# Optimization experiments

Hardware: AMD Instinct MI355X
Metric: run time of the kernel (lower is better)

Reference implementation:

```python
import jax, jax.numpy as jnp
import numpy as np

N = 4096
DK = 128   # d_k == d_e == d_h (required by gate shapes in KAG)
DH = 128
DR = 64
DE = 128
NHEADS = 3
ALPHA = 0.2
NEG_INF = -9e15


def _xavier(k, shape, gain=1.414):
    fan_in, fan_out = shape[-2], shape[-1]
    limit = gain * np.sqrt(6.0 / (fan_in + fan_out))
    return jax.random.uniform(k, shape, minval=-limit, maxval=limit, dtype=jnp.float32)


def setup_inputs() -> dict:
    key = jax.random.key(0)
    ks = jax.random.split(key, 16)
    x = jax.random.normal(ks[0], (N, DK), dtype=jnp.float32)
    adj = (jax.random.uniform(ks[1], (N, N)) < 0.01).astype(jnp.float32)
    adj = jnp.maximum(adj, jnp.eye(N, dtype=jnp.float32))
    e_t = jax.random.normal(ks[2], (N, DE), dtype=jnp.float32)
    r_t = jax.random.normal(ks[3], (N, DR), dtype=jnp.float32)
    prev_h = jax.random.normal(ks[4], (N, DH), dtype=jnp.float32)
    # GAT params: NHEADS input heads + one output head
    W_heads = _xavier(ks[5], (NHEADS, DK, DH))
    a_heads = _xavier(ks[6], (NHEADS, 2 * DH, 1))
    W_out = _xavier(ks[7], (NHEADS * DH, DH))
    a_out = _xavier(ks[8], (2 * DH, 1))
    # KAG + OutputLayer linear params (stored [in, out])
    din_kag = DK + DR + DH  # 320
    Wq_w = _xavier(ks[9], (din_kag, DK), gain=1.0)
    Wq_b = jnp.zeros((DK,), jnp.float32)
    Wh_w = _xavier(ks[10], (din_kag, DH), gain=1.0)
    Wh_b = jnp.zeros((DH,), jnp.float32)
    din_out = DK + DE + DH  # 384
    Wp_w = _xavier(ks[11], (din_out, DH), gain=1.0)
    Wp_b = jnp.zeros((DH,), jnp.float32)
    return {"x": x, "adj": adj, "e_t": e_t, "r_t": r_t, "prev_h": prev_h,
            "W_heads": W_heads, "a_heads": a_heads, "W_out": W_out, "a_out": a_out,
            "Wq_w": Wq_w, "Wq_b": Wq_b, "Wh_w": Wh_w, "Wh_b": Wh_b,
            "Wp_w": Wp_w, "Wp_b": Wp_b}


def _gat_layer(h, adj, W, a, concat):
    # h: [N, Fin], W: [Fin, F], a: [2F, 1]
    Wh = h @ W                       # [N, F]
    F_ = W.shape[1]
    # a^T [Wh_i ; Wh_j] == (Wh a1)_i + (Wh a2)_j  -- identical math, no [N,N,2F]
    f1 = Wh @ a[:F_]                 # [N, 1]
    f2 = Wh @ a[F_:]                 # [N, 1]
    e = jax.nn.leaky_relu(f1 + f2.T, negative_slope=ALPHA)  # [N, N]
    e = jnp.where(adj > 0, e, NEG_INF)
    att = jax.nn.softmax(e, axis=1)  # dropout(p=0.6) is identity in eval mode
    h_prime = att @ Wh               # [N, F]
    return jax.nn.elu(h_prime) if concat else h_prime


def reference(x, adj, e_t, r_t, prev_h, W_heads, a_heads, W_out, a_out,
              Wq_w, Wq_b, Wh_w, Wh_b, Wp_w, Wp_b):
    # --- GAT ---
    heads = jax.vmap(lambda W, a: _gat_layer(x, adj, W, a, True))(W_heads, a_heads)  # [H,N,DH]
    h_cat = jnp.transpose(heads, (1, 0, 2)).reshape(N, NHEADS * DH)
    h_gat = jax.nn.elu(_gat_layer(h_cat, adj, W_out, a_out, False))  # [N, DH]
    # --- KAG gated update (x_t := e_t per CEKT.forward call) ---
    comb = jnp.concatenate([e_t, r_t, prev_h], axis=1)  # [N, DE+DR+DH]
    g = jax.nn.sigmoid(comb @ Wq_w + Wq_b)
    cand = jnp.tanh(comb @ Wh_w + Wh_b)
    h_t = (1.0 - g) * prev_h + g * cand                 # [N, DH]
    # --- Output layer (kc_t := x per CEKT.forward call) ---
    comb2 = jnp.concatenate([h_t, e_t, x], axis=1)      # [N, DH+DE+DK]
    y_t = jax.nn.sigmoid(comb2 @ Wp_w + Wp_b)           # [N, DH]
    return y_t
```

## Files before the change

kernel.cpp:

```cpp
#include <hip/hip_runtime.h>
#include <hip/hip_bf16.h>


typedef short s16x8 __attribute__((ext_vector_type(8)));
typedef float f32x4 __attribute__((ext_vector_type(4)));

constexpr int NKQ = 10;
constexpr int NKP = 12;

__device__ __forceinline__ ushort bf16_rne(float f) {
    union { float f; uint u; } a; a.f = f;
    return (ushort)((a.u + 0x7FFFu + ((a.u >> 16) & 1u)) >> 16);
}
__device__ __forceinline__ float fsigmoid(float z) {
    return 1.0f / (1.0f + __expf(-z));
}
__device__ __forceinline__ float ftanh(float z) {
    const float a = fabsf(z);
    const float t = __expf(-2.0f * a);
    const float r = (1.0f - t) / (1.0f + t);
    return copysignf(r, z);
}

__device__ __forceinline__ s16x8 ldfrag(const float* __restrict__ W,
                                        int s, int krow, int colW) {
    const float* p = W + (s * 32 + krow) * 128 + colW;
    union { ushort u[8]; s16x8 v; } r;
#pragma unroll
    for (int j = 0; j < 8; ++j)
        r.u[j] = bf16_rne(p[j * 128]);
    return r.v;
}

__global__ __launch_bounds__(1024, 1) void cekt_fused(
    const float* __restrict__ x,
    const float* __restrict__ e_t,
    const float* __restrict__ r_t,
    const float* __restrict__ prev_h,
    const float* __restrict__ Wq,
    const float* __restrict__ Wh,
    const float* __restrict__ Wp,
    const float* __restrict__ bq,
    const float* __restrict__ bh,
    const float* __restrict__ bp,
    float* __restrict__ out)
{
    __shared__ alignas(16) ushort A1h[NKQ * 64 * 8];
    __shared__ alignas(16) ushort A2h[NKP * 64 * 8];
    __shared__ f32x4 p1g[8][64], p1c[8][64], p2y[8][64];

    const int t = threadIdx.x;
    const int row0 = blockIdx.x * 16;
    const int w = t >> 6, lane = t & 63;
    const int ct = w & 7, kh = w >> 3;
    const int krow = (lane >> 4) * 8;
    const int colW = ct * 16 + (lane & 15);
    const int colL = lane & 15, rg = lane >> 4;
    const int col = ct * 16 + colL;

    const int sbeg = kh * 5;
    s16x8 hq[5], hc[5];
#pragma unroll
    for (int si = 0; si < 5; ++si) {
        hq[si] = ldfrag(Wq, sbeg + si, krow, colW);
        hc[si] = ldfrag(Wh, sbeg + si, krow, colW);
    }

    for (int i = t; i < 1280; i += 1024) {
        const int row = i / 80, kq4 = i - row * 80;
        const int k0 = kq4 * 4;
        float4 v;
        if (k0 < 128)      v = *(const float4*)&e_t[(row0 + row) * 128 + k0];
        else if (k0 < 192) v = *(const float4*)&r_t[(row0 + row) * 64 + (k0 - 128)];
        else               v = *(const float4*)&prev_h[(row0 + row) * 128 + (k0 - 192)];
        const int s = k0 >> 5, q = (k0 >> 3) & 3, j0 = k0 & 7;
        const int base = (s * 64 + q * 16 + row) * 8 + j0;
        ushort hi4[4];
        hi4[0] = bf16_rne(v.x); hi4[1] = bf16_rne(v.y);
        hi4[2] = bf16_rne(v.z); hi4[3] = bf16_rne(v.w);
        *(uint2*)&A1h[base] = *(const uint2*)hi4;
    }
    {
        const int row = t >> 6, kr = t & 63;
        const int k0 = 128 + kr * 4;
        const float4 v = (k0 < 256)
            ? *(const float4*)&e_t[(row0 + row) * 128 + (k0 - 128)]
            : *(const float4*)&x[(row0 + row) * 128 + (k0 - 256)];
        const int s = k0 >> 5, q = (k0 >> 3) & 3, j0 = k0 & 7;
        const int base = (s * 64 + q * 16 + row) * 8 + j0;
        ushort hi4[4];
        hi4[0] = bf16_rne(v.x); hi4[1] = bf16_rne(v.y);
        hi4[2] = bf16_rne(v.z); hi4[3] = bf16_rne(v.w);
        *(uint2*)&A2h[base] = *(const uint2*)hi4;
    }
    __syncthreads();

    f32x4 gacc = {0, 0, 0, 0}, cacc = {0, 0, 0, 0};
#pragma unroll
    for (int si = 0; si < 5; ++si) {
        const int s = sbeg + si;
        const s16x8 aH = *(const s16x8*)&A1h[(s * 64 + lane) * 8];
        gacc = __builtin_amdgcn_mfma_f32_16x16x32_bf16(aH, hq[si], gacc, 0, 0, 0);
        cacc = __builtin_amdgcn_mfma_f32_16x16x32_bf16(aH, hc[si], cacc, 0, 0, 0);
    }

    s16x8 pH[6];
    float ph4[4];
    if (kh) {
        p1g[ct][lane] = gacc;
        p1c[ct][lane] = cacc;
#pragma unroll
        for (int si = 0; si < 6; ++si)
            pH[si] = ldfrag(Wp, 6 + si, krow, colW);
    } else {
#pragma unroll
        for (int i2 = 0; i2 < 4; ++i2)
            ph4[i2] = prev_h[(row0 + rg * 4 + i2) * 128 + col];
    }
    __syncthreads();

    f32x4 yacc = {0, 0, 0, 0};
    s16x8 rH[6];
    if (!kh) {
#pragma unroll
        for (int si = 0; si < 6; ++si)
            rH[si] = ldfrag(Wp, si, krow, colW);
        gacc += p1g[ct][lane];
        cacc += p1c[ct][lane];
        const float bqv = bq[col], bhv = bh[col];
        const int s_h = col >> 5, q_h = (col >> 3) & 3, j_h = col & 7;
#pragma unroll
        for (int i2 = 0; i2 < 4; ++i2) {
            const int row = rg * 4 + i2;
            const float g = fsigmoid(gacc[i2] + bqv);
            const float cd = ftanh(cacc[i2] + bhv);
            const float h = (1.0f - g) * ph4[i2] + g * cd;
            A2h[(s_h * 64 + q_h * 16 + row) * 8 + j_h] = bf16_rne(h);
        }
    } else {
#pragma unroll
        for (int si = 0; si < 6; ++si) {
            const int s = 6 + si;
            const s16x8 aH = *(const s16x8*)&A2h[(s * 64 + lane) * 8];
            yacc = __builtin_amdgcn_mfma_f32_16x16x32_bf16(aH, pH[si], yacc, 0, 0, 0);
        }
        p2y[ct][lane] = yacc;
    }
    __syncthreads();

    if (!kh) {
        yacc = p2y[ct][lane];
#pragma unroll
        for (int si = 0; si < 6; ++si) {
            const s16x8 aH = *(const s16x8*)&A2h[(si * 64 + lane) * 8];
            yacc = __builtin_amdgcn_mfma_f32_16x16x32_bf16(aH, rH[si], yacc, 0, 0, 0);
        }
        const float bpv = bp[col];
#pragma unroll
        for (int i2 = 0; i2 < 4; ++i2) {
            const int row = rg * 4 + i2;
            out[(row0 + row) * 128 + col] = fsigmoid(yacc[i2] + bpv);
        }
    }
}

extern "C" void kernel_launch(void* const* d_in, const int* in_sizes, int n_in,
                              void* d_out, int out_size, void* d_ws, size_t ws_size,
                              hipStream_t stream) {
    const float* x      = (const float*)d_in[0];
    const float* e_t    = (const float*)d_in[2];
    const float* r_t    = (const float*)d_in[3];
    const float* prev_h = (const float*)d_in[4];
    const float* Wq_w   = (const float*)d_in[9];
    const float* Wq_b   = (const float*)d_in[10];
    const float* Wh_w   = (const float*)d_in[11];
    const float* Wh_b   = (const float*)d_in[12];
    const float* Wp_w   = (const float*)d_in[13];
    const float* Wp_b   = (const float*)d_in[14];
    float* out  = (float*)d_out;

    hipLaunchKernelGGL(cekt_fused, dim3(256), dim3(1024), 0, stream,
                       x, e_t, r_t, prev_h, Wq_w, Wh_w, Wp_w,
                       Wq_b, Wh_b, Wp_b, out);
}
```

Baseline: 14.59 us.

## Split waves into gate and output roles, removing split-K reductions

Reassigns the 16 waves into two roles. Role 0 computes the full K=320 gate/candidate GEMMs and the h_t update. Role 1 computes the whole output GEMM: the e_t/x part first, then the h_t part after a single barrier. This removes the shared-memory partial-sum buffers and one __syncthreads, at the cost of a longer serial MFMA chain and more weight-fragment loads per wave in role 0.

After: 17.50 us. 1.2x slower.

```diff
diff --git a/kernel.cpp b/kernel.cpp
--- a/kernel.cpp
+++ b/kernel.cpp
@@ -47,23 +47,35 @@
 {
     __shared__ alignas(16) ushort A1h[NKQ * 64 * 8];
     __shared__ alignas(16) ushort A2h[NKP * 64 * 8];
-    __shared__ f32x4 p1g[8][64], p1c[8][64], p2y[8][64];
 
     const int t = threadIdx.x;
     const int row0 = blockIdx.x * 16;
     const int w = t >> 6, lane = t & 63;
-    const int ct = w & 7, kh = w >> 3;
+    const int ct = w & 7, role = w >> 3;
     const int krow = (lane >> 4) * 8;
     const int colW = ct * 16 + (lane & 15);
     const int colL = lane & 15, rg = lane >> 4;
     const int col = ct * 16 + colL;
 
-    const int sbeg = kh * 5;
     s16x8 hq[5], hc[5];
+    s16x8 pH[8], rH[4];
+    float ph4[4];
+    if (!role) {
 #pragma unroll
-    for (int si = 0; si < 5; ++si) {
-        hq[si] = ldfrag(Wq, sbeg + si, krow, colW);
-        hc[si] = ldfrag(Wh, sbeg + si, krow, colW);
+        for (int si = 0; si < 5; ++si) {
+            hq[si] = ldfrag(Wq, si, krow, colW);
+            hc[si] = ldfrag(Wh, si, krow, colW);
+        }
+#pragma unroll
+        for (int i2 = 0; i2 < 4; ++i2)
+            ph4[i2] = prev_h[(row0 + rg * 4 + i2) * 128 + col];
+    } else {
+#pragma unroll
+        for (int si = 0; si < 8; ++si)
+            pH[si] = ldfrag(Wp, 4 + si, krow, colW);
+#pragma unroll
+        for (int si = 0; si < 4; ++si)
+            rH[si] = ldfrag(Wp, si, krow, colW);
     }
 
     for (int i = t; i < 1280; i += 1024) {
@@ -95,38 +107,27 @@
     }
     __syncthreads();
 
-    f32x4 gacc = {0, 0, 0, 0}, cacc = {0, 0, 0, 0};
+    f32x4 yacc = {0, 0, 0, 0};
+    if (!role) {
+        s16x8 hq2[5], hc2[5];
 #pragma unroll
-    for (int si = 0; si < 5; ++si) {
-        const int s = sbeg + si;
-        const s16x8 aH = *(const s16x8*)&A1h[(s * 64 + lane) * 8];
-        gacc = __builtin_amdgcn_mfma_f32_16x16x32_bf16(aH, hq[si], gacc, 0, 0, 0);
-        cacc = __builtin_amdgcn_mfma_f32_16x16x32_bf16(aH, hc[si], cacc, 0, 0, 0);
-    }
-
-    s16x8 pH[6];
-    float ph4[4];
-    if (kh) {
-        p1g[ct][lane] = gacc;
-        p1c[ct][lane] = cacc;
+        for (int si = 0; si < 5; ++si) {
+            hq2[si] = ldfrag(Wq, 5 + si, krow, colW);
+            hc2[si] = ldfrag(Wh, 5 + si, krow, colW);
+        }
+        f32x4 gacc = {0, 0, 0, 0}, cacc = {0, 0, 0, 0};
 #pragma unroll
-        for (int si = 0; si < 6; ++si)
-            pH[si] = ldfrag(Wp, 6 + si, krow, colW);
-    } else {
+        for (int si = 0; si < 5; ++si) {
+            const s16x8 aH = *(const s16x8*)&A1h[(si * 64 + lane) * 8];
+            gacc = __builtin_amdgcn_mfma_f32_16x16x32_bf16(aH, hq[si], gacc, 0, 0, 0);
+            cacc = __builtin_amdgcn_mfma_f32_16x16x32_bf16(aH, hc[si], cacc, 0, 0, 0);
+        }
 #pragma unroll
-        for (int i2 = 0; i2 < 4; ++i2)
-            ph4[i2] = prev_h[(row0 + rg * 4 + i2) * 128 + col];
-    }
-    __syncthreads();
-
-    f32x4 yacc = {0, 0, 0, 0};
-    s16x8 rH[6];
-    if (!kh) {
-#pragma unroll
-        for (int si = 0; si < 6; ++si)
-            rH[si] = ldfrag(Wp, si, krow, colW);
-        gacc += p1g[ct][lane];
-        cacc += p1c[ct][lane];
+        for (int si = 0; si < 5; ++si) {
+            const s16x8 aH = *(const s16x8*)&A1h[((5 + si) * 64 + lane) * 8];
+            gacc = __builtin_amdgcn_mfma_f32_16x16x32_bf16(aH, hq2[si], gacc, 0, 0, 0);
+            cacc = __builtin_amdgcn_mfma_f32_16x16x32_bf16(aH, hc2[si], cacc, 0, 0, 0);
+        }
         const float bqv = bq[col], bhv = bh[col];
         const int s_h = col >> 5, q_h = (col >> 3) & 3, j_h = col & 7;
 #pragma unroll
@@ -139,19 +140,16 @@
         }
     } else {
 #pragma unroll
-        for (int si = 0; si < 6; ++si) {
-            const int s = 6 + si;
-            const s16x8 aH = *(const s16x8*)&A2h[(s * 64 + lane) * 8];
+        for (int si = 0; si < 8; ++si) {
+            const s16x8 aH = *(const s16x8*)&A2h[((4 + si) * 64 + lane) * 8];
             yacc = __builtin_amdgcn_mfma_f32_16x16x32_bf16(aH, pH[si], yacc, 0, 0, 0);
         }
-        p2y[ct][lane] = yacc;
     }
     __syncthreads();
 
-    if (!kh) {
-        yacc = p2y[ct][lane];
+    if (role) {
 #pragma unroll
-        for (int si = 0; si < 6; ++si) {
+        for (int si = 0; si < 4; ++si) {
             const s16x8 aH = *(const s16x8*)&A2h[(si * 64 + lane) * 8];
             yacc = __builtin_amdgcn_mfma_f32_16x16x32_bf16(aH, rH[si], yacc, 0, 0, 0);
         }
```
